# Kernel tuning notes

Measured on AMD Instinct MI355X. Metric: run time of the kernel, lower is better.

The kernel has to match this reference:

```python
import jax, jax.numpy as jnp
import numpy as np

N_NODES = 50000
N_EDGES = 800000
K = 15          # kernel points
P_DIM = 3
IN_DIM = 32
OUT_DIM = 64
KP_EXTENT = 0.6


def setup_inputs() -> dict:
    key = jax.random.key(0)
    k1, k2, k3, k4, k5, k6 = jax.random.split(key, 6)
    pos = jax.random.normal(k1, (N_NODES, P_DIM), dtype=jnp.float32)
    feat = jax.random.normal(k2, (N_NODES, IN_DIM), dtype=jnp.float32)
    # kernel point layout inside a ball of the given radius (load_kernels stand-in)
    kernel_points = jax.random.normal(k3, (K, P_DIM), dtype=jnp.float32) * 0.5
    kernel_points = kernel_points.at[0].set(0.0)  # fixed center point
    weights = jax.random.normal(k4, (K, IN_DIM, OUT_DIM), dtype=jnp.float32) * (1.0 / np.sqrt(IN_DIM))
    edge_src = jax.random.randint(k5, (N_EDGES,), 0, N_NODES, dtype=jnp.int32)
    edge_dst = jax.random.randint(k6, (N_EDGES,), 0, N_NODES, dtype=jnp.int32)
    return {"pos": pos, "feat": feat, "kernel_points": kernel_points,
            "weights": weights, "edge_src": edge_src, "edge_dst": edge_dst}


def reference(pos, feat, kernel_points, weights, edge_src, edge_dst):
    n_nodes = pos.shape[0]
    # per-edge relative position: src - dst  [E, p]
    y = pos[edge_src] - pos[edge_dst]
    # distance to each kernel point  [E, k]
    diff = y[:, None, :] - kernel_points[None, :, :]
    dist = jnp.sqrt(jnp.sum(diff * diff, axis=-1))
    # linear correlation influence  [E, k]
    m = jax.nn.relu(1.0 - dist / KP_EXTENT)
    # per-edge weighted features  [E, k, in]
    f = feat[edge_src]
    contrib = m[:, :, None] * f[:, None, :]
    # segment-reduce onto destination nodes  [N, k, in]
    weighted_f = jax.ops.segment_sum(contrib, edge_dst, num_segments=n_nodes)
    # per-kernel-point matmul and sum over kernel points  [N, out]
    return jnp.einsum('nki,kio->no', weighted_f, weights)
```

## Files before the change

kernel.cpp:

```cpp
#include <hip/hip_runtime.h>
#include <hip/hip_fp16.h>

#define N_NODES 50000
#define N_EDGES 800000
#define KPTS 15
#define IN_DIM 32
#define OUT_DIM 64
#define KP_EXTENT 0.6f
#define INV_EXT (1.0f / KP_EXTENT)
#define EXT2 (KP_EXTENT * KP_EXTENT)

#define CAP 131072
#define NREP 16
#define SEG_CAP (CAP / NREP)
#define CNT_STRIDE 32
#define K1_BLOCKS (N_EDGES / 256)
#define SUBB 16

#define PCNT_OFF 32768
#define FEATH_OFF (1u << 20)
#define LIST_OFF  (8u << 20)
#define SLOT_OFF  (32u << 20)
#define SCAP_MAX 16

typedef unsigned int uint;

#define RFL(x) ((uint)__builtin_amdgcn_readfirstlane((int)(x)))

static __device__ __forceinline__ float h2f16(uint u) {
    return __half2float(__ushort_as_half((unsigned short)(u & 0xffffu)));
}
static __device__ __forceinline__ uint pack2(float lo, float hi) {
    return (uint)__half_as_ushort(__float2half_rn(lo))
         | ((uint)__half_as_ushort(__float2half_rn(hi)) << 16);
}

#if __has_builtin(__builtin_amdgcn_fdot2)
typedef _Float16 h2v __attribute__((ext_vector_type(2)));
static __device__ __forceinline__ float fdot2u(uint a, uint b, float c) {
    union U { uint u; h2v h; };
    U ua, ub; ua.u = a; ub.u = b;
    return __builtin_amdgcn_fdot2(ua.h, ub.h, c, false);
}
#else
static __device__ __forceinline__ float fdot2u(uint a, uint b, float c) {
    const float al = h2f16(a), ah = h2f16(a >> 16);
    const float bl = h2f16(b), bh = h2f16(b >> 16);
    return fmaf(ah, bh, fmaf(al, bl, c));
}
#endif

__global__ __launch_bounds__(256) void geom_compact(
    const float* __restrict__ pos,
    const float* __restrict__ feat,
    const float* __restrict__ kp,
    const int*   __restrict__ esrc,
    const int*   __restrict__ edst,
    int*         __restrict__ cnt,
    int*         __restrict__ pcnt,
    uint2*       __restrict__ lists,
    uint*        __restrict__ featH,
    float4*      __restrict__ outz,
    uint*        __restrict__ slots16,
    const int scap)
{
    __shared__ int s_wavecnt[KPTS][4];
    __shared__ int s_woff[KPTS][4];
    __shared__ int s_base[KPTS];

    const int tid  = threadIdx.x;
    const int wv   = tid >> 6;
    const int lane = tid & 63;
    const int rep  = blockIdx.x & (NREP - 1);

    const int e = blockIdx.x * 256 + tid;

    outz[e] = make_float4(0.0f, 0.0f, 0.0f, 0.0f);
    {
        const float2 fv = ((const float2*)feat)[e];
        featH[e] = pack2(fv.x, fv.y);
    }

    const int s = esrc[e];
    const int d = edst[e];

    const float yx = pos[s * 3 + 0] - pos[d * 3 + 0];
    const float yy = pos[s * 3 + 1] - pos[d * 3 + 1];
    const float yz = pos[s * 3 + 2] - pos[d * 3 + 2];

    float d2v[KPTS];
    unsigned act = 0;
    #pragma unroll
    for (int k = 0; k < KPTS; ++k) {
        const float dx = yx - kp[k * 3 + 0];
        const float dy = yy - kp[k * 3 + 1];
        const float dz = yz - kp[k * 3 + 2];
        const float d2 = dx * dx + dy * dy + dz * dz;
        d2v[k] = d2;
        if (d2 < EXT2) act |= (1u << k);
    }

    const int nact = __popc(act);
    int ti = 0;
    if (nact > 0) ti = atomicAdd(pcnt + d, nact);

    unsigned long long kmask[KPTS];
    #pragma unroll
    for (int k = 0; k < KPTS; ++k) {
        kmask[k] = __ballot((act >> k) & 1u);
        if (lane == 0) s_wavecnt[k][wv] = __popcll(kmask[k]);
    }
    __syncthreads();

    if (tid < KPTS) {
        int o0 = 0;
        #pragma unroll
        for (int w = 0; w < 4; ++w) {
            s_woff[tid][w] = o0;
            o0 += s_wavecnt[tid][w];
        }
        s_base[tid] = (o0 > 0)
            ? atomicAdd(&cnt[(tid * NREP + rep) * CNT_STRIDE], o0) : 0;
    }
    __syncthreads();

    const unsigned long long lt = (lane == 63) ? 0x7fffffffffffffffull
                                               : ((1ull << lane) - 1ull);
    #pragma unroll
    for (int k = 0; k < KPTS; ++k) {
        const unsigned long long mask = kmask[k];
        if (mask == 0ull) continue;
        if ((act >> k) & 1u) {
            const int rank = __popcll(mask & lt);
            const int idx  = s_base[k] + s_woff[k][wv] + rank;

            const int t = ti;
            ++ti;
            const unsigned ey = (t < scap)
                ? (unsigned)((d * scap + t) * OUT_DIM)
                : (0x80000000u | (unsigned)d);

            if (idx < SEG_CAP) {
                const float mk = 1.0f - sqrtf(d2v[k]) * INV_EXT;
                const unsigned mh =
                    (unsigned)__half_as_ushort(__float2half(mk));
                lists[(size_t)k * CAP + (size_t)rep * SEG_CAP + idx] =
                    make_uint2(((unsigned)s << 16) | mh, ey);
            } else if (!(ey & 0x80000000u)) {
                uint* row = slots16 + (ey >> 1);
                #pragma unroll
                for (int j = 0; j < OUT_DIM / 2; ++j) row[j] = 0u;
            }
        }
    }
}

__global__ __launch_bounds__(256) void pair_matmul(
    const uint*  __restrict__ featH,
    const float* __restrict__ W,
    const int*   __restrict__ cnt,
    const uint2* __restrict__ lists,
    float*       __restrict__ out,
    uint*        __restrict__ slots16)
{
    const int seg  = blockIdx.x % (KPTS * NREP);
    const int sub  = blockIdx.x / (KPTS * NREP);
    const int k    = seg >> 4;
    const int rep  = seg & (NREP - 1);
    const int wv   = threadIdx.x >> 6;
    const int lane = threadIdx.x & 63;

    uint wpk[16];
    #pragma unroll
    for (int j = 0; j < 16; ++j) {
        const float wa = W[k * (IN_DIM * OUT_DIM) + (2 * j)     * OUT_DIM + lane];
        const float wb = W[k * (IN_DIM * OUT_DIM) + (2 * j + 1) * OUT_DIM + lane];
        wpk[j] = pack2(wa, wb);
    }
    #pragma unroll
    for (int j = 0; j < 16; ++j)
        asm volatile("" : "+v"(wpk[j]));

    int n = cnt[seg * CNT_STRIDE];
    if (n > SEG_CAP) n = SEG_CAP;
    const uint2* __restrict__ list =
        lists + (size_t)k * CAP + (size_t)rep * SEG_CAP;

    const int widx    = sub * 4 + wv;
    const int stride2 = SUBB * 4 * 2;

    int base = widx * 2;
    if (base >= n) return;

    uint4 eeA = *reinterpret_cast<const uint4*>(list + base);
    const int bB0 = base + stride2;
    uint4 eeB = *reinterpret_cast<const uint4*>(list + (bB0 < n ? bB0 : 0));

    uint axA0 = RFL(eeA.x), ayA0 = RFL(eeA.y),
         axA1 = RFL(eeA.z), ayA1 = RFL(eeA.w);
    uint sA0 = axA0 >> 16; if (sA0 >= N_NODES) sA0 = 0;
    uint sA1 = axA1 >> 16; if (sA1 >= N_NODES) sA1 = 0;
    uint faA[16], fbA[16];
    {
        const uint* __restrict__ p0 = featH + sA0 * 16;
        const uint* __restrict__ p1 = featH + sA1 * 16;
        #pragma unroll
        for (int j = 0; j < 16; ++j) { faA[j] = p0[j]; fbA[j] = p1[j]; }
    }

    for (; base < n; base += stride2) {
        const int bC = base + 2 * stride2;
        const uint4 eeC = *reinterpret_cast<const uint4*>(list + (bC < n ? bC : 0));

        const uint axB0 = RFL(eeB.x), ayB0 = RFL(eeB.y),
                   axB1 = RFL(eeB.z), ayB1 = RFL(eeB.w);
        uint sB0 = axB0 >> 16; if (sB0 >= N_NODES) sB0 = 0;
        uint sB1 = axB1 >> 16; if (sB1 >= N_NODES) sB1 = 0;
        uint faB[16], fbB[16];
        {
            const uint* __restrict__ p0 = featH + sB0 * 16;
            const uint* __restrict__ p1 = featH + sB1 * 16;
            #pragma unroll
            for (int j = 0; j < 16; ++j) { faB[j] = p0[j]; fbB[j] = p1[j]; }
        }

        float acc0 = 0.0f, acc1 = 0.0f;
        #pragma unroll
        for (int j = 0; j < 16; ++j) {
            acc0 = fdot2u(faA[j], wpk[j], acc0);
            acc1 = fdot2u(fbA[j], wpk[j], acc1);
        }
        const float m0 = h2f16(axA0);
        const float m1 = h2f16(axA1);
        const float r0 = m0 * acc0;
        const float r1 = m1 * acc1;
        const bool  two = (base + 1 < n);

        const float p0 = __shfl_xor(r0, 1);
        const float p1 = __shfl_xor(r1, 1);

        if (!(ayA0 & 0x80000000u)) {
            if (!(lane & 1))
                slots16[(ayA0 >> 1) + (lane >> 1)] = pack2(r0, p0);
        } else {
            atomicAdd(out + (size_t)(ayA0 & 0xffffu) * OUT_DIM + lane, r0);
        }
        if (two) {
            if (!(ayA1 & 0x80000000u)) {
                if (!(lane & 1))
                    slots16[(ayA1 >> 1) + (lane >> 1)] = pack2(r1, p1);
            } else {
                atomicAdd(out + (size_t)(ayA1 & 0xffffu) * OUT_DIM + lane, r1);
            }
        }

        axA0 = axB0; ayA0 = ayB0; axA1 = axB1; ayA1 = ayB1;
        #pragma unroll
        for (int j = 0; j < 16; ++j) { faA[j] = faB[j]; fbA[j] = fbB[j]; }
        eeB = eeC;
    }
}

__global__ __launch_bounds__(256) void node_reduce(
    const int*  __restrict__ pcnt,
    const uint* __restrict__ slots16,
    float*      __restrict__ out,
    const int scap)
{
    const int wv   = threadIdx.x >> 6;
    const int lane = threadIdx.x & 63;
    const int node = blockIdx.x * 8 + wv * 2 + (lane >> 5);
    const int l    = lane & 31;

    const int raw = pcnt[node];
    int deg = raw;
    if (deg > scap) deg = scap;

    const uint* __restrict__ sp =
        slots16 + (size_t)node * ((size_t)scap * 32) + l;

    float a0 = 0.0f, a1 = 0.0f, b0 = 0.0f, b1 = 0.0f;
    int j = 0;
    for (; j + 1 < deg; j += 2) {
        const uint u0 = sp[(size_t)j * 32];
        const uint u1 = sp[(size_t)(j + 1) * 32];
        a0 += h2f16(u0); a1 += h2f16(u0 >> 16);
        b0 += h2f16(u1); b1 += h2f16(u1 >> 16);
    }
    if (j < deg) {
        const uint u0 = sp[(size_t)j * 32];
        a0 += h2f16(u0); a1 += h2f16(u0 >> 16);
    }

    float o0 = a0 + b0;
    float o1 = a1 + b1;
    if (raw > scap) {
        const float2 prev = ((const float2*)out)[(size_t)node * 32 + l];
        o0 += prev.x; o1 += prev.y;
    }
    ((float2*)out)[(size_t)node * 32 + l] = make_float2(o0, o1);
}

extern "C" void kernel_launch(void* const* d_in, const int* in_sizes, int n_in,
                              void* d_out, int out_size, void* d_ws, size_t ws_size,
                              hipStream_t stream)
{
    const float* pos  = (const float*)d_in[0];
    const float* feat = (const float*)d_in[1];
    const float* kp   = (const float*)d_in[2];
    const float* W    = (const float*)d_in[3];
    const int* esrc   = (const int*)d_in[4];
    const int* edst   = (const int*)d_in[5];
    float* out        = (float*)d_out;

    int*   cnt     = (int*)d_ws;
    int*   pcnt    = (int*)((char*)d_ws + PCNT_OFF);
    uint*  featH   = (uint*)((char*)d_ws + FEATH_OFF);
    uint2* lists   = (uint2*)((char*)d_ws + LIST_OFF);
    uint*  slots16 = (uint*)((char*)d_ws + SLOT_OFF);

    const size_t layer_bytes = (size_t)N_NODES * OUT_DIM * 2;
    int scap = 0;
    if (ws_size >= (size_t)SLOT_OFF + layer_bytes) {
        scap = (int)((ws_size - (size_t)SLOT_OFF) / layer_bytes);
        if (scap > SCAP_MAX) scap = SCAP_MAX;
    }

    hipMemsetAsync(d_ws, 0, 262144, stream);

    geom_compact<<<K1_BLOCKS, 256, 0, stream>>>(pos, feat, kp, esrc, edst,
                                                cnt, pcnt, lists, featH,
                                                (float4*)out, slots16, scap);
    pair_matmul<<<SUBB * KPTS * NREP, 256, 0, stream>>>(featH, W, cnt, lists,
                                                        out, slots16);
    if (scap > 0)
        node_reduce<<<N_NODES / 8, 256, 0, stream>>>(pcnt, slots16, out, scap);
}
```

Baseline: 126.6 us.

## Use MFMA 16x16x32 f16 for per-pair feature-weight matmul in pair_matmul

Replaces the per-lane fdot2 loop, which handled two edge pairs per wavefront iteration, with MFMA 16x16x32 f16 instructions. Each wavefront now processes 16 pairs at once against a 32x64 weight tile held in registers. It also halves the sub-block count (SUBB 16 to 8) and drops the software prefetch pipeline. Results are scattered as half stores with 16-column strides, or as atomics, which may make the writes less coalesced than the packed 32-bit stores used before.

```diff
diff --git a/kernel.cpp b/kernel.cpp
--- a/kernel.cpp
+++ b/kernel.cpp
@@ -15,7 +15,8 @@
 #define SEG_CAP (CAP / NREP)
 #define CNT_STRIDE 32
 #define K1_BLOCKS (N_EDGES / 256)
-#define SUBB 16
+#define SUBB 8
+#define WPS (SUBB * 4)
 
 #define PCNT_OFF 32768
 #define FEATH_OFF (1u << 20)
@@ -24,8 +25,10 @@
 #define SCAP_MAX 16
 
 typedef unsigned int uint;
-
-#define RFL(x) ((uint)__builtin_amdgcn_readfirstlane((int)(x)))
+typedef _Float16 f16x8 __attribute__((ext_vector_type(8)));
+typedef float f32x4 __attribute__((ext_vector_type(4)));
+
+union FU { uint u[4]; f16x8 h; };
 
 static __device__ __forceinline__ float h2f16(uint u) {
     return __half2float(__ushort_as_half((unsigned short)(u & 0xffffu)));
@@ -34,21 +37,6 @@
     return (uint)__half_as_ushort(__float2half_rn(lo))
          | ((uint)__half_as_ushort(__float2half_rn(hi)) << 16);
 }
-
-#if __has_builtin(__builtin_amdgcn_fdot2)
-typedef _Float16 h2v __attribute__((ext_vector_type(2)));
-static __device__ __forceinline__ float fdot2u(uint a, uint b, float c) {
-    union U { uint u; h2v h; };
-    U ua, ub; ua.u = a; ub.u = b;
-    return __builtin_amdgcn_fdot2(ua.h, ub.h, c, false);
-}
-#else
-static __device__ __forceinline__ float fdot2u(uint a, uint b, float c) {
-    const float al = h2f16(a), ah = h2f16(a >> 16);
-    const float bl = h2f16(b), bh = h2f16(b >> 16);
-    return fmaf(ah, bh, fmaf(al, bl, c));
-}
-#endif
 
 __global__ __launch_bounds__(256) void geom_compact(
     const float* __restrict__ pos,
@@ -169,95 +157,85 @@
     const int rep  = seg & (NREP - 1);
     const int wv   = threadIdx.x >> 6;
     const int lane = threadIdx.x & 63;
-
-    uint wpk[16];
-    #pragma unroll
-    for (int j = 0; j < 16; ++j) {
-        const float wa = W[k * (IN_DIM * OUT_DIM) + (2 * j)     * OUT_DIM + lane];
-        const float wb = W[k * (IN_DIM * OUT_DIM) + (2 * j + 1) * OUT_DIM + lane];
-        wpk[j] = pack2(wa, wb);
-    }
-    #pragma unroll
-    for (int j = 0; j < 16; ++j)
-        asm volatile("" : "+v"(wpk[j]));
+    const int col  = lane & 15;
+    const int grp  = lane >> 4;
+
+    uint bu[4][4];
+    const float* __restrict__ Wk = W + k * (IN_DIM * OUT_DIM);
+    #pragma unroll
+    for (int t = 0; t < 4; ++t) {
+        #pragma unroll
+        for (int j = 0; j < 4; ++j) {
+            const int kk = grp * 8 + 2 * j;
+            const float wa = Wk[kk * OUT_DIM + t * 16 + col];
+            const float wb = Wk[(kk + 1) * OUT_DIM + t * 16 + col];
+            bu[t][j] = pack2(wa, wb);
+        }
+    }
+    #pragma unroll
+    for (int t = 0; t < 4; ++t)
+        #pragma unroll
+        for (int j = 0; j < 4; ++j)
+            asm volatile("" : "+v"(bu[t][j]));
 
     int n = cnt[seg * CNT_STRIDE];
     if (n > SEG_CAP) n = SEG_CAP;
     const uint2* __restrict__ list =
         lists + (size_t)k * CAP + (size_t)rep * SEG_CAP;
-
-    const int widx    = sub * 4 + wv;
-    const int stride2 = SUBB * 4 * 2;
-
-    int base = widx * 2;
-    if (base >= n) return;
-
-    uint4 eeA = *reinterpret_cast<const uint4*>(list + base);
-    const int bB0 = base + stride2;
-    uint4 eeB = *reinterpret_cast<const uint4*>(list + (bB0 < n ? bB0 : 0));
-
-    uint axA0 = RFL(eeA.x), ayA0 = RFL(eeA.y),
-         axA1 = RFL(eeA.z), ayA1 = RFL(eeA.w);
-    uint sA0 = axA0 >> 16; if (sA0 >= N_NODES) sA0 = 0;
-    uint sA1 = axA1 >> 16; if (sA1 >= N_NODES) sA1 = 0;
-    uint faA[16], fbA[16];
-    {
-        const uint* __restrict__ p0 = featH + sA0 * 16;
-        const uint* __restrict__ p1 = featH + sA1 * 16;
+    const int nsteps = (n + 15) >> 4;
+
+    const int w = sub * 4 + wv;
+    for (int s = w; s < nsteps; s += WPS) {
+        const int pi = s * 16 + col;
+        const uint2 ent = (pi < n) ? list[pi] : make_uint2(0u, 0xFFFFFFFFu);
+
+        const uint src = ent.x >> 16;
+        FU A;
+        {
+            const uint* __restrict__ fp = featH + src * 16 + grp * 4;
+            #pragma unroll
+            for (int j = 0; j < 4; ++j) A.u[j] = fp[j];
+        }
+        const float mym = h2f16(ent.x);
+
+        f32x4 C0 = {0,0,0,0}, C1 = {0,0,0,0}, C2 = {0,0,0,0}, C3 = {0,0,0,0};
+        {
+            FU b0, b1, b2, b3;
+            #pragma unroll
+            for (int j = 0; j < 4; ++j) {
+                b0.u[j] = bu[0][j]; b1.u[j] = bu[1][j];
+                b2.u[j] = bu[2][j]; b3.u[j] = bu[3][j];
+            }
+            C0 = __builtin_amdgcn_mfma_f32_16x16x32_f16(A.h, b0.h, C0, 0, 0, 0);
+            C1 = __builtin_amdgcn_mfma_f32_16x16x32_f16(A.h, b1.h, C1, 0, 0, 0);
+            C2 = __builtin_amdgcn_mfma_f32_16x16x32_f16(A.h, b2.h, C2, 0, 0, 0);
+            C3 = __builtin_amdgcn_mfma_f32_16x16x32_f16(A.h, b3.h, C3, 0, 0, 0);
+        }
+
         #pragma unroll
-        for (int j = 0; j < 16; ++j) { faA[j] = p0[j]; fbA[j] = p1[j]; }
-    }
-
-    for (; base < n; base += stride2) {
-        const int bC = base + 2 * stride2;
-        const uint4 eeC = *reinterpret_cast<const uint4*>(list + (bC < n ? bC : 0));
-
-        const uint axB0 = RFL(eeB.x), ayB0 = RFL(eeB.y),
-                   axB1 = RFL(eeB.z), ayB1 = RFL(eeB.w);
-        uint sB0 = axB0 >> 16; if (sB0 >= N_NODES) sB0 = 0;
-        uint sB1 = axB1 >> 16; if (sB1 >= N_NODES) sB1 = 0;
-        uint faB[16], fbB[16];
-        {
-            const uint* __restrict__ p0 = featH + sB0 * 16;
-            const uint* __restrict__ p1 = featH + sB1 * 16;
-            #pragma unroll
-            for (int j = 0; j < 16; ++j) { faB[j] = p0[j]; fbB[j] = p1[j]; }
-        }
-
-        float acc0 = 0.0f, acc1 = 0.0f;
-        #pragma unroll
-        for (int j = 0; j < 16; ++j) {
-            acc0 = fdot2u(faA[j], wpk[j], acc0);
-            acc1 = fdot2u(fbA[j], wpk[j], acc1);
-        }
-        const float m0 = h2f16(axA0);
-        const float m1 = h2f16(axA1);
-        const float r0 = m0 * acc0;
-        const float r1 = m1 * acc1;
-        const bool  two = (base + 1 < n);
-
-        const float p0 = __shfl_xor(r0, 1);
-        const float p1 = __shfl_xor(r1, 1);
-
-        if (!(ayA0 & 0x80000000u)) {
-            if (!(lane & 1))
-                slots16[(ayA0 >> 1) + (lane >> 1)] = pack2(r0, p0);
-        } else {
-            atomicAdd(out + (size_t)(ayA0 & 0xffffu) * OUT_DIM + lane, r0);
-        }
-        if (two) {
-            if (!(ayA1 & 0x80000000u)) {
-                if (!(lane & 1))
-                    slots16[(ayA1 >> 1) + (lane >> 1)] = pack2(r1, p1);
+        for (int i = 0; i < 4; ++i) {
+            const int r = grp * 4 + i;
+            const float mr = __shfl(mym, r);
+            const uint  er = (uint)__shfl((int)ent.y, r);
+            if (er == 0xFFFFFFFFu) continue;
+            const float v0 = mr * C0[i];
+            const float v1 = mr * C1[i];
+            const float v2 = mr * C2[i];
+            const float v3 = mr * C3[i];
+            if (!(er & 0x80000000u)) {
+                __half* __restrict__ sp = (__half*)slots16 + (size_t)er + col;
+                sp[0]  = __float2half_rn(v0);
+                sp[16] = __float2half_rn(v1);
+                sp[32] = __float2half_rn(v2);
+                sp[48] = __float2half_rn(v3);
             } else {
-                atomicAdd(out + (size_t)(ayA1 & 0xffffu) * OUT_DIM + lane, r1);
+                float* __restrict__ op = out + (size_t)(er & 0xffffu) * OUT_DIM + col;
+                atomicAdd(op +  0, v0);
+                atomicAdd(op + 16, v1);
+                atomicAdd(op + 32, v2);
+                atomicAdd(op + 48, v3);
             }
         }
-
-        axA0 = axB0; ayA0 = ayB0; axA1 = axB1; ayA1 = ayB1;
-        #pragma unroll
-        for (int j = 0; j < 16; ++j) { faA[j] = faB[j]; fbA[j] = fbB[j]; }
-        eeB = eeC;
     }
 }
 
```

Result: faster. 114.6 us (-9.5%).
